# Kernel tuning notes

Hardware: AMD Instinct MI355X
Metric: run time of the kernel (lower is better)

## Reference

```python
import jax, jax.numpy as jnp
import numpy as np
import math

IN_FEATURES = 729   # n^2 with n = 27 = 3^3
HIDDEN = 2916
OUT_FEATURES = 729
BASE = 3
FACTOR = 0
B, D = 64, 768      # batch, channel dim (x: [B, D, IN_FEATURES])


def _butterfly_factor_to_matrix(twiddle, factor_index):
    # twiddle: (n//b, b, b) -> dense n x n butterfly factor matrix (numpy, setup-time only)
    n_div_b, b, _ = twiddle.shape
    n = b * n_div_b
    stride = b ** factor_index
    # eye(n) rearranged: 'bs (diagblk j stride)' -> (bs, diagblk, j, stride)
    x = np.eye(n, dtype=np.float32).reshape(n, n // (b * stride), b, stride)
    # twiddle rearranged: '(diagblk stride) i j' -> (diagblk, stride, i, j)
    t = twiddle.reshape(n // (b * stride), stride, b, b)
    out = np.einsum('dsij,bdjs->bdis', t, x).reshape(n, n)
    return out.T


def _sparse_mask():
    b = BASE
    log_b_n = int(math.log(math.sqrt(IN_FEATURES), b))
    n = b ** log_b_n
    twiddle = np.arange(1, n * b + 1, dtype=np.float32).reshape(n // b, b, b)
    m1 = _butterfly_factor_to_matrix(twiddle, FACTOR)
    mask = np.kron(m1, m1)
    return jnp.asarray((mask > 0).astype(np.float32))  # [729, 729] 0/1 mask


def setup_inputs() -> dict:
    key = jax.random.key(0)
    k1, k2, k3, k4 = jax.random.split(key, 4)
    x = jax.random.normal(k1, (B, D, IN_FEATURES), jnp.float32)
    w1 = jax.random.normal(k2, (HIDDEN, IN_FEATURES), jnp.float32) / math.sqrt(IN_FEATURES)
    w2 = jax.random.normal(k3, (OUT_FEATURES, HIDDEN), jnp.float32) / math.sqrt(HIDDEN)
    b2 = jax.random.normal(k4, (OUT_FEATURES,), jnp.float32) * 0.01
    return {"x": x, "w1": w1, "w2": w2, "b2": b2, "sparse_mask": _sparse_mask()}


def reference(x, w1, w2, b2, sparse_mask):
    # attn_s[s,t] = sum_d fc1.W[d,s] * fc2.W[t,d], then butterfly-masked
    attn = jnp.einsum('ds,td->st', w1, w2) * sparse_mask  # [in, out]
    out = jnp.einsum('bds,st->bdt', x, attn) + b2          # [B, D, out]
    return jax.nn.gelu(out, approximate=False)             # torch nn.GELU uses exact erf
```

## Files before the change

### kernel.cpp

```cpp
#include <hip/hip_runtime.h>
#include <hip/hip_bf16.h>


__device__ __forceinline__ float gelu_f(float v) {
    float u2 = v * v;
    float z = -1.5957691216f * v * fmaf(0.044715f, u2, 1.0f);
    float e = __expf(z);
    return v * __builtin_amdgcn_rcpf(1.0f + e);
}

__global__ void attn_zero_kernel(float* __restrict__ attn) {
    int i = blockIdx.x * 256 + threadIdx.x;
    if (i < 81 * 81) attn[i] = 0.0f;
}

#define CH 108

__global__ __launch_bounds__(256) void bfly_attn_kernel(
        const float* __restrict__ w1,
        const float* __restrict__ w2,
        float* __restrict__ attn)
{
    const int G1    = blockIdx.x % 9;
    const int d0    = (blockIdx.x / 9) * CH;
    const int tid   = threadIdx.x;

    __shared__ float ws1[CH * 81];
    __shared__ float ws2[81 * CH];

    for (int i = tid; i < CH * 81; i += 256) {
        int dl = i / 81, c = i % 81;
        ws1[i] = w1[(d0 + dl) * 729 + 81 * G1 + c];
    }
    for (int i = tid; i < 81 * CH; i += 256) {
        int tl = i / CH, dl = i % CH;
        ws2[i] = w2[(81 * G1 + tl) * 2916 + d0 + dl];
    }
    __syncthreads();

    if (tid < 243) {
        const int G2  = tid / 27;
        const int ls  = (tid % 27) / 3;
        const int lt0 = (tid % 3) * 3;
        const int s_l = 27 * (ls / 3) + 3 * G2 + (ls % 3);
        int t_l[3];
        #pragma unroll
        for (int j = 0; j < 3; ++j) {
            int lt = lt0 + j;
            t_l[j] = 27 * (lt / 3) + 3 * G2 + (lt % 3);
        }

        float a0 = 0.f, a1 = 0.f, a2 = 0.f;
        for (int dl = 0; dl < CH; ++dl) {
            float av = ws1[dl * 81 + s_l];
            a0 = fmaf(av, ws2[t_l[0] * CH + dl], a0);
            a1 = fmaf(av, ws2[t_l[1] * CH + dl], a1);
            a2 = fmaf(av, ws2[t_l[2] * CH + dl], a2);
        }

        const int g = 9 * G1 + G2;
        float* dst = &attn[g * 81 + ls * 9 + lt0];
        atomicAdd(dst + 0, a0);
        atomicAdd(dst + 1, a1);
        atomicAdd(dst + 2, a2);
    }
}

#define ROWS 8

struct f3 { float x, y, z; };

__global__ __launch_bounds__(256) void bfly_mlp_kernel(
        const float* __restrict__ xg,
        const float* __restrict__ attn,
        const float* __restrict__ b2g,
        float* __restrict__ outg)
{
    const int tid = threadIdx.x;
    if (tid >= 243) return;

    const int t1 = tid / 9;
    const int G2 = tid % 9;
    const int G1 = t1 / 3;
    const int li = t1 % 3;
    const int tb = 3 * tid;
    const int sb = 81 * G1 + 3 * G2;
    const int g  = 9 * G1 + G2;

    float a[9][3], bias[3];
    #pragma unroll
    for (int ls = 0; ls < 9; ++ls) {
        f3 v = *reinterpret_cast<const f3*>(&attn[g * 81 + ls * 9 + 3 * li]);
        a[ls][0] = v.x; a[ls][1] = v.y; a[ls][2] = v.z;
    }
    {
        f3 v = *reinterpret_cast<const f3*>(&b2g[tb]);
        bias[0] = v.x; bias[1] = v.y; bias[2] = v.z;
    }

    const long long rowbase = (long long)blockIdx.x * ROWS;
    const float* __restrict__ xbase = xg + rowbase * 729 + sb;

    #pragma unroll 2
    for (int r = 0; r < ROWS; ++r) {
        const float* xr = xbase + (long long)r * 729;
        f3 v0 = *reinterpret_cast<const f3*>(xr);
        f3 v1 = *reinterpret_cast<const f3*>(xr + 27);
        f3 v2 = *reinterpret_cast<const f3*>(xr + 54);
        float xv[9] = { v0.x, v0.y, v0.z, v1.x, v1.y, v1.z, v2.x, v2.y, v2.z };

        float acc0 = bias[0], acc1 = bias[1], acc2 = bias[2];
        #pragma unroll
        for (int ls = 0; ls < 9; ++ls) {
            acc0 = fmaf(xv[ls], a[ls][0], acc0);
            acc1 = fmaf(xv[ls], a[ls][1], acc1);
            acc2 = fmaf(xv[ls], a[ls][2], acc2);
        }

        f3 o; o.x = gelu_f(acc0); o.y = gelu_f(acc1); o.z = gelu_f(acc2);
        *reinterpret_cast<f3*>(&outg[(rowbase + r) * 729 + tb]) = o;
    }
}

extern "C" void kernel_launch(void* const* d_in, const int* in_sizes, int n_in,
                              void* d_out, int out_size, void* d_ws, size_t ws_size,
                              hipStream_t stream) {
    const float* x  = (const float*)d_in[0];
    const float* w1 = (const float*)d_in[1];
    const float* w2 = (const float*)d_in[2];
    const float* b2 = (const float*)d_in[3];

    float* attn = (float*)d_ws;

    attn_zero_kernel<<<26, 256, 0, stream>>>(attn);
    bfly_attn_kernel<<<9 * 27, 256, 0, stream>>>(w1, w2, attn);

    const int n_rows = 64 * 768;
    bfly_mlp_kernel<<<n_rows / ROWS, 256, 0, stream>>>(
        x, attn, b2, (float*)d_out);
}
```

Measured before the change: 280.9 us.

## Software-pipeline row loads in MLP kernel and halve attn reduction chunk

The MLP kernel now handles 32 rows per block (1536 blocks) with a double-buffered register pipeline: the next 4-row chunk of x is loaded while the current chunk is computed and stored, with sched barriers keeping the loads hoisted. Launch bounds now request 4 waves per EU. The attn precompute chunk shrinks from 108 to 54, doubling its block count to spread the reduction over more CUs at the cost of more atomics. The aim is to hide global memory latency in the bandwidth-bound main kernel, while the extra x registers may raise register pressure.

```diff
diff --git a/kernel.cpp b/kernel.cpp
--- a/kernel.cpp
+++ b/kernel.cpp
@@ -14,7 +14,7 @@
     if (i < 81 * 81) attn[i] = 0.0f;
 }
 
-#define CH 108
+#define CH 54
 
 __global__ __launch_bounds__(256) void bfly_attn_kernel(
         const float* __restrict__ w1,
@@ -66,11 +66,13 @@
     }
 }
 
-#define ROWS 8
+#define RPC 4
+#define CPB 8
+#define NBLK 1536
 
 struct f3 { float x, y, z; };
 
-__global__ __launch_bounds__(256) void bfly_mlp_kernel(
+__global__ __launch_bounds__(256, 4) void bfly_mlp_kernel(
         const float* __restrict__ xg,
         const float* __restrict__ attn,
         const float* __restrict__ b2g,
@@ -98,27 +100,54 @@
         bias[0] = v.x; bias[1] = v.y; bias[2] = v.z;
     }
 
-    const long long rowbase = (long long)blockIdx.x * ROWS;
+    const long long rowbase = (long long)blockIdx.x * (RPC * CPB);
     const float* __restrict__ xbase = xg + rowbase * 729 + sb;
+    float* __restrict__ obase       = outg + rowbase * 729 + tb;
 
-    #pragma unroll 2
-    for (int r = 0; r < ROWS; ++r) {
-        const float* xr = xbase + (long long)r * 729;
-        f3 v0 = *reinterpret_cast<const f3*>(xr);
-        f3 v1 = *reinterpret_cast<const f3*>(xr + 27);
-        f3 v2 = *reinterpret_cast<const f3*>(xr + 54);
-        float xv[9] = { v0.x, v0.y, v0.z, v1.x, v1.y, v1.z, v2.x, v2.y, v2.z };
+    float xa[RPC][9], xb[RPC][9];
 
-        float acc0 = bias[0], acc1 = bias[1], acc2 = bias[2];
+    auto load_chunk = [&](int c, float (&dst)[RPC][9]) {
         #pragma unroll
-        for (int ls = 0; ls < 9; ++ls) {
-            acc0 = fmaf(xv[ls], a[ls][0], acc0);
-            acc1 = fmaf(xv[ls], a[ls][1], acc1);
-            acc2 = fmaf(xv[ls], a[ls][2], acc2);
+        for (int r = 0; r < RPC; ++r) {
+            const float* xr = xbase + (c * RPC + r) * 729;
+            f3 v0 = *reinterpret_cast<const f3*>(xr);
+            f3 v1 = *reinterpret_cast<const f3*>(xr + 27);
+            f3 v2 = *reinterpret_cast<const f3*>(xr + 54);
+            dst[r][0] = v0.x; dst[r][1] = v0.y; dst[r][2] = v0.z;
+            dst[r][3] = v1.x; dst[r][4] = v1.y; dst[r][5] = v1.z;
+            dst[r][6] = v2.x; dst[r][7] = v2.y; dst[r][8] = v2.z;
         }
+    };
 
-        f3 o; o.x = gelu_f(acc0); o.y = gelu_f(acc1); o.z = gelu_f(acc2);
-        *reinterpret_cast<f3*>(&outg[(rowbase + r) * 729 + tb]) = o;
+    auto comp_store = [&](int c, const float (&src)[RPC][9]) {
+        #pragma unroll
+        for (int r = 0; r < RPC; ++r) {
+            float acc0 = bias[0], acc1 = bias[1], acc2 = bias[2];
+            #pragma unroll
+            for (int ls = 0; ls < 9; ++ls) {
+                acc0 = fmaf(src[r][ls], a[ls][0], acc0);
+                acc1 = fmaf(src[r][ls], a[ls][1], acc1);
+                acc2 = fmaf(src[r][ls], a[ls][2], acc2);
+            }
+            f3 o; o.x = gelu_f(acc0); o.y = gelu_f(acc1); o.z = gelu_f(acc2);
+            *reinterpret_cast<f3*>(obase + (c * RPC + r) * 729) = o;
+        }
+    };
+
+    load_chunk(0, xa);
+    __builtin_amdgcn_sched_barrier(0x7);
+
+    #pragma unroll
+    for (int c = 0; c < CPB; c += 2) {
+        load_chunk(c + 1, xb);
+        __builtin_amdgcn_sched_barrier(0x7);
+        comp_store(c, xa);
+
+        if (c + 2 < CPB) {
+            load_chunk(c + 2, xa);
+            __builtin_amdgcn_sched_barrier(0x7);
+        }
+        comp_store(c + 1, xb);
     }
 }
 
@@ -133,9 +162,7 @@
     float* attn = (float*)d_ws;
 
     attn_zero_kernel<<<26, 256, 0, stream>>>(attn);
-    bfly_attn_kernel<<<9 * 27, 256, 0, stream>>>(w1, w2, attn);
+    bfly_attn_kernel<<<9 * (2916 / CH), 256, 0, stream>>>(w1, w2, attn);
 
-    const int n_rows = 64 * 768;
-    bfly_mlp_kernel<<<n_rows / ROWS, 256, 0, stream>>>(
-        x, attn, b2, (float*)d_out);
+    bfly_mlp_kernel<<<NBLK, 256, 0, stream>>>(x, attn, b2, (float*)d_out);
 }
```

New measurement: 295.1 us. 5.1% more time.
